# Optimization experiments

Hardware: AMD Instinct MI355X
Metric: run time of the kernel (lower is better)

The kernel has to match this reference:

```python
import jax, jax.numpy as jnp
import numpy as np

N = 131072   # number of profile points
S = 64       # n_samples (PSF samples per point)
D = H = W = 256


def setup_inputs() -> dict:
    key = jax.random.key(0)
    k1, k2, k3, k4, k5, k6 = jax.random.split(key, 6)
    x = jax.random.normal(k1, (1, 1, D, H, W), dtype=jnp.float32)
    # voxel-space coordinates (x, y, z) inside the volume
    sampleGrid = jax.random.uniform(k2, (N, 3), dtype=jnp.float32) * jnp.array(
        [W - 1, H - 1, D - 1], dtype=jnp.float32)
    # small axis-angle rotations + translations: [N, 1, 6]
    rot = jax.random.normal(k3, (N, 1, 3), dtype=jnp.float32) * 0.02
    trn = jax.random.normal(k4, (N, 1, 3), dtype=jnp.float32) * 2.0
    ax = jnp.concatenate([rot, trn], axis=-1)
    half = jax.random.uniform(k5, (N, 1, 3), minval=1.0, maxval=3.0, dtype=jnp.float32)
    bound = jnp.concatenate([-half, half], axis=1)  # [N, 2, 3]
    InvCovScaled = jnp.eye(3, dtype=jnp.float32) * 0.5
    # torch.randn(...) - 0.5 from the original forward, hoisted out for determinism
    xyz_psf = jax.random.normal(k6, (N, S, 3), dtype=jnp.float32) - 0.5
    return dict(x=x, sampleGrid=sampleGrid, ax=ax, bound=bound,
                InvCovScaled=InvCovScaled, xyz_psf=xyz_psf)


def _axisangle2mat(a):
    # a: [N, 6] -> [N, 3, 4] = [R | t] via Rodrigues
    v, t = a[:, :3], a[:, 3:]
    theta = jnp.linalg.norm(v, axis=-1, keepdims=True)          # [N,1]
    k = v / jnp.maximum(theta, 1e-12)                            # unit axis
    kx, ky, kz = k[:, 0], k[:, 1], k[:, 2]
    z = jnp.zeros_like(kx)
    K = jnp.stack([z, -kz, ky, kz, z, -kx, -ky, kx, z], axis=-1).reshape(-1, 3, 3)
    ct = jnp.cos(theta)[..., None]  # [N,1,1]
    st = jnp.sin(theta)[..., None]
    I = jnp.eye(3, dtype=a.dtype)
    R = I + st * K + (1.0 - ct) * jnp.matmul(K, K)
    return jnp.concatenate([R, t[..., None]], axis=-1)           # [N,3,4]


def _grid_sample_3d(vol, grid):
    # vol: [D,H,W]; grid: [M,3] normalized coords (x,y,z) in [-1,1]
    # matches F.grid_sample(mode='bilinear', padding_mode='zeros', align_corners=False)
    d, h, w = vol.shape
    sizes = jnp.array([w, h, d], dtype=vol.dtype)
    pix = ((grid + 1.0) * sizes - 1.0) * 0.5                     # unnormalize
    ix, iy, iz = pix[:, 0], pix[:, 1], pix[:, 2]
    x0 = jnp.floor(ix); y0 = jnp.floor(iy); z0 = jnp.floor(iz)
    fx = ix - x0; fy = iy - y0; fz = iz - z0
    x0 = x0.astype(jnp.int32); y0 = y0.astype(jnp.int32); z0 = z0.astype(jnp.int32)

    def gather(xi, yi, zi):
        valid = ((xi >= 0) & (xi < w) & (yi >= 0) & (yi < h) & (zi >= 0) & (zi < d))
        xc = jnp.clip(xi, 0, w - 1)
        yc = jnp.clip(yi, 0, h - 1)
        zc = jnp.clip(zi, 0, d - 1)
        return jnp.where(valid, vol[zc, yc, xc], jnp.zeros((), vol.dtype))

    out = jnp.zeros(grid.shape[0], dtype=vol.dtype)
    for dx in (0, 1):
        wx = fx if dx else (1.0 - fx)
        for dy in (0, 1):
            wy = fy if dy else (1.0 - fy)
            for dz in (0, 1):
                wz = fz if dz else (1.0 - fz)
                out = out + gather(x0 + dx, y0 + dy, z0 + dz) * (wx * wy * wz)
    return out


def reference(x, sampleGrid, ax, bound, InvCovScaled, xyz_psf):
    vol = x[0, 0]                                                # [D,H,W]
    size = jnp.array([x.shape[-1], x.shape[-2], x.shape[-3]], dtype=x.dtype)  # [W,H,D]

    # pose matrices [N,1,3,4]
    mat = _axisangle2mat(ax.reshape(-1, 6)).reshape(ax.shape[:-1] + (3, 4))
    R = mat[..., :3]                                             # [N,1,3,3]
    T = mat[..., 3]                                              # [N,1,3]
    # trans_first=True: p' = R @ (p + T)
    p = sampleGrid[:, None] + T                                  # [N,1,3]
    mat_sampleGrid = jnp.einsum('nkij,nkj->nki', R, p)           # [N,1,3]

    # PSF offsets: [N,S,3]
    bound_psf = xyz_psf * ((bound[:, 1, :] - bound[:, 0, :]) * 0.5)[:, None]
    psf = mat_sampleGrid + bound_psf                             # [N,S,3]

    grid = 2.0 * (psf / (size - 1.0) - 0.5)                      # normalize per-axis
    psf_x = _grid_sample_3d(vol, grid.reshape(-1, 3)).reshape(psf.shape[:-1])  # [N,S]

    center = bound_psf
    q = jnp.einsum('nsi,ij,nsj->ns', center, InvCovScaled, center)
    w = jnp.exp(-0.5 * q)                                        # [N,S]
    y = (psf_x * w).sum(-1) / w.sum(-1)                          # [N]
    return y
```

## Files before the change

### kernel.cpp

```cpp
#include <hip/hip_runtime.h>


#define VOL_N 256
#define S_PSF 64
#define NBUCKET 4096
#define TBL_ELEMS (1 << 24)
#define TBL_BYTES ((size_t)TBL_ELEMS * 8)

typedef float vf4 __attribute__((ext_vector_type(4)));
typedef _Float16 vh4 __attribute__((ext_vector_type(4)));
typedef _Float16 vh8 __attribute__((ext_vector_type(8)));


__device__ __forceinline__ int bucket_of(const float* __restrict__ sg, int n) {
    int cx = min(max((int)sg[n * 3 + 0], 0), VOL_N - 1) >> 4;
    int cy = min(max((int)sg[n * 3 + 1], 0), VOL_N - 1) >> 4;
    int cz = min(max((int)sg[n * 3 + 2], 0), VOL_N - 1) >> 4;
    int m = 0;
    #pragma unroll
    for (int b = 0; b < 4; b++) {
        m |= (((cx >> b) & 1) << (3 * b))
           | (((cy >> b) & 1) << (3 * b + 1))
           | (((cz >> b) & 1) << (3 * b + 2));
    }
    return m;
}

__global__ void zero_hist_kernel(int* __restrict__ ws) {
    int i = blockIdx.x * blockDim.x + threadIdx.x;
    if (i < NBUCKET) ws[i] = 0;
}

__global__ void hist_kernel(const float* __restrict__ sg, int* __restrict__ ws, int N) {
    int n = blockIdx.x * blockDim.x + threadIdx.x;
    if (n >= N) return;
    atomicAdd(&ws[bucket_of(sg, n)], 1);
}

__global__ __launch_bounds__(1024) void scan_kernel(int* __restrict__ ws) {
    __shared__ int tmp[1024];
    const int t = threadIdx.x;
    int h0 = ws[t * 4 + 0], h1 = ws[t * 4 + 1], h2 = ws[t * 4 + 2], h3 = ws[t * 4 + 3];
    int s = h0 + h1 + h2 + h3;
    tmp[t] = s;
    __syncthreads();
    for (int off = 1; off < 1024; off <<= 1) {
        int v = (t >= off) ? tmp[t - off] : 0;
        __syncthreads();
        tmp[t] += v;
        __syncthreads();
    }
    int excl = tmp[t] - s;
    ws[NBUCKET + t * 4 + 0] = excl;
    ws[NBUCKET + t * 4 + 1] = excl + h0;
    ws[NBUCKET + t * 4 + 2] = excl + h0 + h1;
    ws[NBUCKET + t * 4 + 3] = excl + h0 + h1 + h2;
}

__global__ void scatter_kernel(const float* __restrict__ sg,
                               const float* __restrict__ ax,
                               const float* __restrict__ bound,
                               int* __restrict__ ws,
                               float* __restrict__ pre, int N) {
    int n = blockIdx.x * blockDim.x + threadIdx.x;
    if (n >= N) return;
    int b = bucket_of(sg, n);
    int pos = atomicAdd(&ws[NBUCKET + b], 1);
    ws[2 * NBUCKET + pos] = n;

    const float vx = ax[n * 6 + 0], vy = ax[n * 6 + 1], vz = ax[n * 6 + 2];
    const float tx = ax[n * 6 + 3], ty = ax[n * 6 + 4], tz = ax[n * 6 + 5];

    const float theta = sqrtf(vx * vx + vy * vy + vz * vz);
    const float kinv = 1.0f / fmaxf(theta, 1e-12f);
    const float kx = vx * kinv, ky = vy * kinv, kz = vz * kinv;
    const float ct = __cosf(theta), st = __sinf(theta);
    const float oc = 1.0f - ct;

    const float r00 = 1.0f + oc * (-(ky * ky + kz * kz));
    const float r01 = -st * kz + oc * kx * ky;
    const float r02 =  st * ky + oc * kx * kz;
    const float r10 =  st * kz + oc * kx * ky;
    const float r11 = 1.0f + oc * (-(kx * kx + kz * kz));
    const float r12 = -st * kx + oc * ky * kz;
    const float r20 = -st * ky + oc * kx * kz;
    const float r21 =  st * kx + oc * ky * kz;
    const float r22 = 1.0f + oc * (-(kx * kx + ky * ky));

    const float px = sg[n * 3 + 0] + tx;
    const float py = sg[n * 3 + 1] + ty;
    const float pz = sg[n * 3 + 2] + tz;

    const float cx = r00 * px + r01 * py + r02 * pz;
    const float cy = r10 * px + r11 * py + r12 * pz;
    const float cz = r20 * px + r21 * py + r22 * pz;

    const float hx = (bound[n * 6 + 3] - bound[n * 6 + 0]) * 0.5f;
    const float hy = (bound[n * 6 + 4] - bound[n * 6 + 1]) * 0.5f;
    const float hz = (bound[n * 6 + 5] - bound[n * 6 + 2]) * 0.5f;

    const float scale = (float)VOL_N / (float)(VOL_N - 1);
    float4 A = make_float4(cx * scale - 0.5f, cy * scale - 0.5f,
                           cz * scale - 0.5f, hx);
    float4 B = make_float4(hy, hz, 0.0f, 0.0f);
    *(float4*)(pre + (size_t)pos * 8)     = A;
    *(float4*)(pre + (size_t)pos * 8 + 4) = B;
}

__global__ __launch_bounds__(256) void build_quad_kernel(
    const float* __restrict__ vol, vh4* __restrict__ tbl) {
    const int t = blockIdx.x * 256 + threadIdx.x;
    const int x2 = (t & 127) << 1;
    const int y = (t >> 7) & 255;
    const int z = t >> 15;
    const float* r0 = vol + (z << 16) + (y << 8);
    const float* r1 = vol + (z << 16) + (min(y + 1, VOL_N - 1) << 8);
    const float2 a = *(const float2*)(r0 + x2);
    const float2 b = *(const float2*)(r1 + x2);
    const float a2 = (x2 == VOL_N - 2) ? a.y : r0[x2 + 2];
    const float b2 = (x2 == VOL_N - 2) ? b.y : r1[x2 + 2];

    union { vh8 h; vf4 f; } o;
    o.h = (vh8){(_Float16)a.x, (_Float16)a.y, (_Float16)b.x, (_Float16)b.y,
                (_Float16)a.y, (_Float16)a2,  (_Float16)b.y, (_Float16)b2};
    *(vf4*)(tbl + ((z << 16) + (y << 8) + x2)) = o.f;
}

template <bool USE_TBL, bool USE_PRE>
__global__ __launch_bounds__(256, 4) void psf_sample_kernel(
    const float* __restrict__ vol,
    const vh4* __restrict__ tbl,
    const float* __restrict__ sampleGrid,
    const float* __restrict__ ax,
    const float* __restrict__ bound,
    const float* __restrict__ invcov,
    const float* __restrict__ xyz_psf,
    const int* __restrict__ perm,
    const float* __restrict__ pre,
    float* __restrict__ out,
    int N)
{
    const int lane = threadIdx.x & 63;

    int bid = blockIdx.x;
    const int nb = gridDim.x;
    if ((nb & 7) == 0) bid = (bid & 7) * (nb >> 3) + (bid >> 3);

    const int ii = bid * (blockDim.x >> 6) + (threadIdx.x >> 6);
    if (ii >= N) return;
    const int i = __builtin_amdgcn_readfirstlane(ii);
    const int n = USE_PRE ? __builtin_amdgcn_readfirstlane(perm[i]) : i;

    const float scale = (float)VOL_N / (float)(VOL_N - 1);
    float icx, icy, icz, hx, hy, hz;
    if (USE_PRE) {
        const float4 A = *(const float4*)(pre + (size_t)i * 8);
        const float4 B = *(const float4*)(pre + (size_t)i * 8 + 4);
        icx = A.x; icy = A.y; icz = A.z; hx = A.w; hy = B.x; hz = B.y;
    } else {
        const float vx = ax[n * 6 + 0], vy = ax[n * 6 + 1], vz = ax[n * 6 + 2];
        const float tx = ax[n * 6 + 3], ty = ax[n * 6 + 4], tz = ax[n * 6 + 5];
        const float theta = sqrtf(vx * vx + vy * vy + vz * vz);
        const float kinv = 1.0f / fmaxf(theta, 1e-12f);
        const float kx = vx * kinv, ky = vy * kinv, kz = vz * kinv;
        const float ct = __cosf(theta), st = __sinf(theta);
        const float oc = 1.0f - ct;
        const float r00 = 1.0f + oc * (-(ky * ky + kz * kz));
        const float r01 = -st * kz + oc * kx * ky;
        const float r02 =  st * ky + oc * kx * kz;
        const float r10 =  st * kz + oc * kx * ky;
        const float r11 = 1.0f + oc * (-(kx * kx + kz * kz));
        const float r12 = -st * kx + oc * ky * kz;
        const float r20 = -st * ky + oc * kx * kz;
        const float r21 =  st * kx + oc * ky * kz;
        const float r22 = 1.0f + oc * (-(kx * kx + ky * ky));
        const float px = sampleGrid[n * 3 + 0] + tx;
        const float py = sampleGrid[n * 3 + 1] + ty;
        const float pz = sampleGrid[n * 3 + 2] + tz;
        icx = (r00 * px + r01 * py + r02 * pz) * scale - 0.5f;
        icy = (r10 * px + r11 * py + r12 * pz) * scale - 0.5f;
        icz = (r20 * px + r21 * py + r22 * pz) * scale - 0.5f;
        hx = (bound[n * 6 + 3] - bound[n * 6 + 0]) * 0.5f;
        hy = (bound[n * 6 + 4] - bound[n * 6 + 1]) * 0.5f;
        hz = (bound[n * 6 + 5] - bound[n * 6 + 2]) * 0.5f;
    }

    const float m00 = invcov[0], m01 = invcov[1], m02 = invcov[2];
    const float m10 = invcov[3], m11 = invcov[4], m12 = invcov[5];
    const float m20 = invcov[6], m21 = invcov[7], m22 = invcov[8];

    const int pbase = (n * S_PSF + lane) * 3;
    const float gx = __builtin_nontemporal_load(xyz_psf + pbase + 0);
    const float gy = __builtin_nontemporal_load(xyz_psf + pbase + 1);
    const float gz = __builtin_nontemporal_load(xyz_psf + pbase + 2);
    const float ox = gx * hx, oy = gy * hy, oz = gz * hz;

    const float ix = fmaf(ox, scale, icx);
    const float iy = fmaf(oy, scale, icy);
    const float iz = fmaf(oz, scale, icz);

    const float x0f = floorf(ix), y0f = floorf(iy), z0f = floorf(iz);
    const float fx = ix - x0f, fy = iy - y0f, fz = iz - z0f;
    const int x0 = (int)x0f, y0 = (int)y0f, z0 = (int)z0f;

    const float wx0 = ((unsigned)x0       < (unsigned)VOL_N) ? (1.0f - fx) : 0.0f;
    const float wx1 = ((unsigned)(x0 + 1) < (unsigned)VOL_N) ? fx          : 0.0f;
    const float wy0 = ((unsigned)y0       < (unsigned)VOL_N) ? (1.0f - fy) : 0.0f;
    const float wy1 = ((unsigned)(y0 + 1) < (unsigned)VOL_N) ? fy          : 0.0f;
    const float wz0 = ((unsigned)z0       < (unsigned)VOL_N) ? (1.0f - fz) : 0.0f;
    const float wz1 = ((unsigned)(z0 + 1) < (unsigned)VOL_N) ? fz          : 0.0f;

    float v000, v001, v010, v011, v100, v101, v110, v111;
    if (USE_TBL) {
        const int xg = min(max(x0, 0), VOL_N - 1);
        const int yg = min(max(y0, 0), VOL_N - 1);
        const int zg0 = min(max(z0, 0), VOL_N - 1);
        const int zg1 = min(max(z0 + 1, 0), VOL_N - 1);
        const int common = (yg << 8) + xg;
        const vh4 p0 = tbl[(zg0 << 16) + common];
        const vh4 p1 = tbl[(zg1 << 16) + common];
        const bool lox = x0 < 0;
        const bool loy = y0 < 0;
        float s00 = p0.x, s01 = p0.y, s10 = p0.z, s11 = p0.w;
        float a01 = lox ? s00 : s01, a11 = lox ? s10 : s11;
        v000 = s00;                 v001 = a01;
        v010 = loy ? s00 : s10;     v011 = loy ? a01 : a11;
        s00 = p1.x; s01 = p1.y; s10 = p1.z; s11 = p1.w;
        a01 = lox ? s00 : s01; a11 = lox ? s10 : s11;
        v100 = s00;                 v101 = a01;
        v110 = loy ? s00 : s10;     v111 = loy ? a01 : a11;
    } else {
        const int xc0 = min(max(x0, 0), VOL_N - 1);
        const int xc1 = min(max(x0 + 1, 0), VOL_N - 1);
        const int yc0 = min(max(y0, 0), VOL_N - 1);
        const int yc1 = min(max(y0 + 1, 0), VOL_N - 1);
        const int zc0 = min(max(z0, 0), VOL_N - 1);
        const int zc1 = min(max(z0 + 1, 0), VOL_N - 1);
        const int zo0 = zc0 << 16, zo1 = zc1 << 16;
        const int yo0 = yc0 << 8, yo1 = yc1 << 8;
        v000 = vol[zo0 + yo0 + xc0];
        v001 = vol[zo0 + yo0 + xc1];
        v010 = vol[zo0 + yo1 + xc0];
        v011 = vol[zo0 + yo1 + xc1];
        v100 = vol[zo1 + yo0 + xc0];
        v101 = vol[zo1 + yo0 + xc1];
        v110 = vol[zo1 + yo1 + xc0];
        v111 = vol[zo1 + yo1 + xc1];
    }

    const float r0 = fmaf(v001, wx1, v000 * wx0);
    const float r1 = fmaf(v011, wx1, v010 * wx0);
    const float r2 = fmaf(v101, wx1, v100 * wx0);
    const float r3 = fmaf(v111, wx1, v110 * wx0);
    const float s0 = fmaf(r1, wy1, r0 * wy0);
    const float s1 = fmaf(r3, wy1, r2 * wy0);
    const float acc = fmaf(s1, wz1, s0 * wz0);

    const float qx = fmaf(m00, ox, fmaf(m01, oy, m02 * oz));
    const float qy = fmaf(m10, ox, fmaf(m11, oy, m12 * oz));
    const float qz = fmaf(m20, ox, fmaf(m21, oy, m22 * oz));
    const float q = fmaf(ox, qx, fmaf(oy, qy, oz * qz));
    const float w = __expf(-0.5f * q);

    float num = acc * w;
    float den = w;
    #pragma unroll
    for (int m = 32; m >= 1; m >>= 1) {
        num += __shfl_xor(num, m, 64);
        den += __shfl_xor(den, m, 64);
    }
    if (lane == 0) out[n] = num / den;
}

extern "C" void kernel_launch(void* const* d_in, const int* in_sizes, int n_in,
                              void* d_out, int out_size, void* d_ws, size_t ws_size,
                              hipStream_t stream) {
    const float* x        = (const float*)d_in[0];
    const float* sg       = (const float*)d_in[1];
    const float* ax       = (const float*)d_in[2];
    const float* bound    = (const float*)d_in[3];
    const float* invcov   = (const float*)d_in[4];
    const float* xyz_psf  = (const float*)d_in[5];
    float* out            = (float*)d_out;

    const int N = in_sizes[1] / 3;
    const size_t sort_bytes = (size_t)(2 * NBUCKET + N) * sizeof(int);
    const size_t sort_pad   = (sort_bytes + 31) & ~(size_t)31;
    const size_t pre_bytes  = (size_t)N * 8 * sizeof(float);

    const bool use_tbl  = ws_size >= TBL_BYTES + sort_pad + pre_bytes;
    const bool use_sort = use_tbl || ws_size >= sort_pad + pre_bytes;

    vh4* tbl = use_tbl ? (vh4*)d_ws : nullptr;
    char* base = (char*)d_ws + (use_tbl ? TBL_BYTES : 0);
    int* sort_ws = (int*)base;
    float* pre = (float*)(base + sort_pad);

    int* perm = nullptr;
    if (use_sort) {
        zero_hist_kernel<<<(NBUCKET + 255) / 256, 256, 0, stream>>>(sort_ws);
        hist_kernel<<<(N + 255) / 256, 256, 0, stream>>>(sg, sort_ws, N);
        scan_kernel<<<1, 1024, 0, stream>>>(sort_ws);
        scatter_kernel<<<(N + 255) / 256, 256, 0, stream>>>(sg, ax, bound, sort_ws, pre, N);
        perm = sort_ws + 2 * NBUCKET;
    }
    if (use_tbl) {
        build_quad_kernel<<<(VOL_N * VOL_N * VOL_N / 2) / 256, 256, 0, stream>>>(x, tbl);
    }

    dim3 block(256);
    dim3 grid((N + 3) / 4);
    if (use_tbl) {
        psf_sample_kernel<true, true><<<grid, block, 0, stream>>>(
            x, tbl, sg, ax, bound, invcov, xyz_psf, perm, pre, out, N);
    } else if (use_sort) {
        psf_sample_kernel<false, true><<<grid, block, 0, stream>>>(
            x, nullptr, sg, ax, bound, invcov, xyz_psf, perm, pre, out, N);
    } else {
        psf_sample_kernel<false, false><<<grid, block, 0, stream>>>(
            x, nullptr, sg, ax, bound, invcov, xyz_psf, nullptr, nullptr, out, N);
    }
}
```

Baseline: 304.3 us.

## Process four points per wavefront with 16 lanes each and vectorised PSF loads

```diff
diff --git a/kernel.cpp b/kernel.cpp
--- a/kernel.cpp
+++ b/kernel.cpp
@@ -126,13 +126,10 @@
     *(vf4*)(tbl + ((z << 16) + (y << 8) + x2)) = o.f;
 }
 
-template <bool USE_TBL, bool USE_PRE>
-__global__ __launch_bounds__(256, 4) void psf_sample_kernel(
+template <bool USE_TBL>
+__global__ __launch_bounds__(256, 4) void psf_sample_g4_kernel(
     const float* __restrict__ vol,
     const vh4* __restrict__ tbl,
-    const float* __restrict__ sampleGrid,
-    const float* __restrict__ ax,
-    const float* __restrict__ bound,
     const float* __restrict__ invcov,
     const float* __restrict__ xyz_psf,
     const int* __restrict__ perm,
@@ -141,64 +138,177 @@
     int N)
 {
     const int lane = threadIdx.x & 63;
+    const int g = lane >> 4;
+    const int t = lane & 15;
 
     int bid = blockIdx.x;
     const int nb = gridDim.x;
     if ((nb & 7) == 0) bid = (bid & 7) * (nb >> 3) + (bid >> 3);
 
-    const int ii = bid * (blockDim.x >> 6) + (threadIdx.x >> 6);
-    if (ii >= N) return;
-    const int i = __builtin_amdgcn_readfirstlane(ii);
-    const int n = USE_PRE ? __builtin_amdgcn_readfirstlane(perm[i]) : i;
-
-    const float scale = (float)VOL_N / (float)(VOL_N - 1);
-    float icx, icy, icz, hx, hy, hz;
-    if (USE_PRE) {
-        const float4 A = *(const float4*)(pre + (size_t)i * 8);
-        const float4 B = *(const float4*)(pre + (size_t)i * 8 + 4);
-        icx = A.x; icy = A.y; icz = A.z; hx = A.w; hy = B.x; hz = B.y;
-    } else {
-        const float vx = ax[n * 6 + 0], vy = ax[n * 6 + 1], vz = ax[n * 6 + 2];
-        const float tx = ax[n * 6 + 3], ty = ax[n * 6 + 4], tz = ax[n * 6 + 5];
-        const float theta = sqrtf(vx * vx + vy * vy + vz * vz);
-        const float kinv = 1.0f / fmaxf(theta, 1e-12f);
-        const float kx = vx * kinv, ky = vy * kinv, kz = vz * kinv;
-        const float ct = __cosf(theta), st = __sinf(theta);
-        const float oc = 1.0f - ct;
-        const float r00 = 1.0f + oc * (-(ky * ky + kz * kz));
-        const float r01 = -st * kz + oc * kx * ky;
-        const float r02 =  st * ky + oc * kx * kz;
-        const float r10 =  st * kz + oc * kx * ky;
-        const float r11 = 1.0f + oc * (-(kx * kx + kz * kz));
-        const float r12 = -st * kx + oc * ky * kz;
-        const float r20 = -st * ky + oc * kx * kz;
-        const float r21 =  st * kx + oc * ky * kz;
-        const float r22 = 1.0f + oc * (-(kx * kx + ky * ky));
-        const float px = sampleGrid[n * 3 + 0] + tx;
-        const float py = sampleGrid[n * 3 + 1] + ty;
-        const float pz = sampleGrid[n * 3 + 2] + tz;
-        icx = (r00 * px + r01 * py + r02 * pz) * scale - 0.5f;
-        icy = (r10 * px + r11 * py + r12 * pz) * scale - 0.5f;
-        icz = (r20 * px + r21 * py + r22 * pz) * scale - 0.5f;
-        hx = (bound[n * 6 + 3] - bound[n * 6 + 0]) * 0.5f;
-        hy = (bound[n * 6 + 4] - bound[n * 6 + 1]) * 0.5f;
-        hz = (bound[n * 6 + 5] - bound[n * 6 + 2]) * 0.5f;
-    }
+    const int wave = threadIdx.x >> 6;
+    const int i = (bid * 4 + wave) * 4 + g;
+    const bool valid = i < N;
+    const int ic = valid ? i : 0;
+    const int n = perm[ic];
+
+    const float4 A = *(const float4*)(pre + (size_t)ic * 8);
+    const float4 B = *(const float4*)(pre + (size_t)ic * 8 + 4);
+    const float icx = A.x, icy = A.y, icz = A.z;
+    const float hx = A.w, hy = B.x, hz = B.y;
 
     const float m00 = invcov[0], m01 = invcov[1], m02 = invcov[2];
     const float m10 = invcov[3], m11 = invcov[4], m12 = invcov[5];
     const float m20 = invcov[6], m21 = invcov[7], m22 = invcov[8];
 
+    const float* pp = xyz_psf + ((size_t)n * (S_PSF * 3) + t * 12);
+    const vf4 f0 = __builtin_nontemporal_load((const vf4*)pp);
+    const vf4 f1 = __builtin_nontemporal_load((const vf4*)pp + 1);
+    const vf4 f2 = __builtin_nontemporal_load((const vf4*)pp + 2);
+
+    const float gxx[4] = {f0.x, f0.w, f1.z, f2.y};
+    const float gyy[4] = {f0.y, f1.x, f1.w, f2.z};
+    const float gzz[4] = {f0.z, f1.y, f2.x, f2.w};
+
+    const float scale = (float)VOL_N / (float)(VOL_N - 1);
+    float num = 0.0f, den = 0.0f;
+
+    #pragma unroll
+    for (int k = 0; k < 4; ++k) {
+        const float ox = gxx[k] * hx, oy = gyy[k] * hy, oz = gzz[k] * hz;
+
+        const float ix = fmaf(ox, scale, icx);
+        const float iy = fmaf(oy, scale, icy);
+        const float iz = fmaf(oz, scale, icz);
+
+        const float x0f = floorf(ix), y0f = floorf(iy), z0f = floorf(iz);
+        const float fx = ix - x0f, fy = iy - y0f, fz = iz - z0f;
+        const int x0 = (int)x0f, y0 = (int)y0f, z0 = (int)z0f;
+
+        const float wx0 = ((unsigned)x0       < (unsigned)VOL_N) ? (1.0f - fx) : 0.0f;
+        const float wx1 = ((unsigned)(x0 + 1) < (unsigned)VOL_N) ? fx          : 0.0f;
+        const float wy0 = ((unsigned)y0       < (unsigned)VOL_N) ? (1.0f - fy) : 0.0f;
+        const float wy1 = ((unsigned)(y0 + 1) < (unsigned)VOL_N) ? fy          : 0.0f;
+        const float wz0 = ((unsigned)z0       < (unsigned)VOL_N) ? (1.0f - fz) : 0.0f;
+        const float wz1 = ((unsigned)(z0 + 1) < (unsigned)VOL_N) ? fz          : 0.0f;
+
+        float v000, v001, v010, v011, v100, v101, v110, v111;
+        if (USE_TBL) {
+            const int xg = min(max(x0, 0), VOL_N - 1);
+            const int yg = min(max(y0, 0), VOL_N - 1);
+            const int zg0 = min(max(z0, 0), VOL_N - 1);
+            const int zg1 = min(max(z0 + 1, 0), VOL_N - 1);
+            const int common = (yg << 8) + xg;
+            const vh4 p0 = tbl[(zg0 << 16) + common];
+            const vh4 p1 = tbl[(zg1 << 16) + common];
+            const bool lox = x0 < 0;
+            const bool loy = y0 < 0;
+            float s00 = p0.x, s01 = p0.y, s10 = p0.z, s11 = p0.w;
+            float a01 = lox ? s00 : s01, a11 = lox ? s10 : s11;
+            v000 = s00;                 v001 = a01;
+            v010 = loy ? s00 : s10;     v011 = loy ? a01 : a11;
+            s00 = p1.x; s01 = p1.y; s10 = p1.z; s11 = p1.w;
+            a01 = lox ? s00 : s01; a11 = lox ? s10 : s11;
+            v100 = s00;                 v101 = a01;
+            v110 = loy ? s00 : s10;     v111 = loy ? a01 : a11;
+        } else {
+            const int xc0 = min(max(x0, 0), VOL_N - 1);
+            const int xc1 = min(max(x0 + 1, 0), VOL_N - 1);
+            const int yc0 = min(max(y0, 0), VOL_N - 1);
+            const int yc1 = min(max(y0 + 1, 0), VOL_N - 1);
+            const int zc0 = min(max(z0, 0), VOL_N - 1);
+            const int zc1 = min(max(z0 + 1, 0), VOL_N - 1);
+            const int zo0 = zc0 << 16, zo1 = zc1 << 16;
+            const int yo0 = yc0 << 8, yo1 = yc1 << 8;
+            v000 = vol[zo0 + yo0 + xc0];
+            v001 = vol[zo0 + yo0 + xc1];
+            v010 = vol[zo0 + yo1 + xc0];
+            v011 = vol[zo0 + yo1 + xc1];
+            v100 = vol[zo1 + yo0 + xc0];
+            v101 = vol[zo1 + yo0 + xc1];
+            v110 = vol[zo1 + yo1 + xc0];
+            v111 = vol[zo1 + yo1 + xc1];
+        }
+
+        const float r0 = fmaf(v001, wx1, v000 * wx0);
+        const float r1 = fmaf(v011, wx1, v010 * wx0);
+        const float r2 = fmaf(v101, wx1, v100 * wx0);
+        const float r3 = fmaf(v111, wx1, v110 * wx0);
+        const float s0 = fmaf(r1, wy1, r0 * wy0);
+        const float s1 = fmaf(r3, wy1, r2 * wy0);
+        const float acc = fmaf(s1, wz1, s0 * wz0);
+
+        const float qx = fmaf(m00, ox, fmaf(m01, oy, m02 * oz));
+        const float qy = fmaf(m10, ox, fmaf(m11, oy, m12 * oz));
+        const float qz = fmaf(m20, ox, fmaf(m21, oy, m22 * oz));
+        const float q = fmaf(ox, qx, fmaf(oy, qy, oz * qz));
+        const float w = __expf(-0.5f * q);
+
+        num = fmaf(acc, w, num);
+        den += w;
+    }
+
+    #pragma unroll
+    for (int m = 8; m >= 1; m >>= 1) {
+        num += __shfl_xor(num, m, 64);
+        den += __shfl_xor(den, m, 64);
+    }
+    if (t == 0 && valid) out[n] = num / den;
+}
+
+__global__ __launch_bounds__(256, 4) void psf_sample_plain_kernel(
+    const float* __restrict__ vol,
+    const float* __restrict__ sampleGrid,
+    const float* __restrict__ ax,
+    const float* __restrict__ bound,
+    const float* __restrict__ invcov,
+    const float* __restrict__ xyz_psf,
+    float* __restrict__ out,
+    int N)
+{
+    const int lane = threadIdx.x & 63;
+    const int i = blockIdx.x * (blockDim.x >> 6) + (threadIdx.x >> 6);
+    if (i >= N) return;
+    const int n = __builtin_amdgcn_readfirstlane(i);
+
+    const float vx = ax[n * 6 + 0], vy = ax[n * 6 + 1], vz = ax[n * 6 + 2];
+    const float tx = ax[n * 6 + 3], ty = ax[n * 6 + 4], tz = ax[n * 6 + 5];
+    const float theta = sqrtf(vx * vx + vy * vy + vz * vz);
+    const float kinv = 1.0f / fmaxf(theta, 1e-12f);
+    const float kx = vx * kinv, ky = vy * kinv, kz = vz * kinv;
+    const float ct = __cosf(theta), st = __sinf(theta);
+    const float oc = 1.0f - ct;
+    const float r00 = 1.0f + oc * (-(ky * ky + kz * kz));
+    const float r01 = -st * kz + oc * kx * ky;
+    const float r02 =  st * ky + oc * kx * kz;
+    const float r10 =  st * kz + oc * kx * ky;
+    const float r11 = 1.0f + oc * (-(kx * kx + kz * kz));
+    const float r12 = -st * kx + oc * ky * kz;
+    const float r20 = -st * ky + oc * kx * kz;
+    const float r21 =  st * kx + oc * ky * kz;
+    const float r22 = 1.0f + oc * (-(kx * kx + ky * ky));
+    const float px = sampleGrid[n * 3 + 0] + tx;
+    const float py = sampleGrid[n * 3 + 1] + ty;
+    const float pz = sampleGrid[n * 3 + 2] + tz;
+    const float scale = (float)VOL_N / (float)(VOL_N - 1);
+    const float icx = (r00 * px + r01 * py + r02 * pz) * scale - 0.5f;
+    const float icy = (r10 * px + r11 * py + r12 * pz) * scale - 0.5f;
+    const float icz = (r20 * px + r21 * py + r22 * pz) * scale - 0.5f;
+    const float hx = (bound[n * 6 + 3] - bound[n * 6 + 0]) * 0.5f;
+    const float hy = (bound[n * 6 + 4] - bound[n * 6 + 1]) * 0.5f;
+    const float hz = (bound[n * 6 + 5] - bound[n * 6 + 2]) * 0.5f;
+
+    const float m00 = invcov[0], m01 = invcov[1], m02 = invcov[2];
+    const float m10 = invcov[3], m11 = invcov[4], m12 = invcov[5];
+    const float m20 = invcov[6], m21 = invcov[7], m22 = invcov[8];
+
     const int pbase = (n * S_PSF + lane) * 3;
-    const float gx = __builtin_nontemporal_load(xyz_psf + pbase + 0);
-    const float gy = __builtin_nontemporal_load(xyz_psf + pbase + 1);
-    const float gz = __builtin_nontemporal_load(xyz_psf + pbase + 2);
-    const float ox = gx * hx, oy = gy * hy, oz = gz * hz;
+    const float ox = xyz_psf[pbase + 0] * hx;
+    const float oy = xyz_psf[pbase + 1] * hy;
+    const float oz = xyz_psf[pbase + 2] * hz;
 
     const float ix = fmaf(ox, scale, icx);
     const float iy = fmaf(oy, scale, icy);
     const float iz = fmaf(oz, scale, icz);
-
     const float x0f = floorf(ix), y0f = floorf(iy), z0f = floorf(iz);
     const float fx = ix - x0f, fy = iy - y0f, fz = iz - z0f;
     const int x0 = (int)x0f, y0 = (int)y0f, z0 = (int)z0f;
@@ -210,43 +320,22 @@
     const float wz0 = ((unsigned)z0       < (unsigned)VOL_N) ? (1.0f - fz) : 0.0f;
     const float wz1 = ((unsigned)(z0 + 1) < (unsigned)VOL_N) ? fz          : 0.0f;
 
-    float v000, v001, v010, v011, v100, v101, v110, v111;
-    if (USE_TBL) {
-        const int xg = min(max(x0, 0), VOL_N - 1);
-        const int yg = min(max(y0, 0), VOL_N - 1);
-        const int zg0 = min(max(z0, 0), VOL_N - 1);
-        const int zg1 = min(max(z0 + 1, 0), VOL_N - 1);
-        const int common = (yg << 8) + xg;
-        const vh4 p0 = tbl[(zg0 << 16) + common];
-        const vh4 p1 = tbl[(zg1 << 16) + common];
-        const bool lox = x0 < 0;
-        const bool loy = y0 < 0;
-        float s00 = p0.x, s01 = p0.y, s10 = p0.z, s11 = p0.w;
-        float a01 = lox ? s00 : s01, a11 = lox ? s10 : s11;
-        v000 = s00;                 v001 = a01;
-        v010 = loy ? s00 : s10;     v011 = loy ? a01 : a11;
-        s00 = p1.x; s01 = p1.y; s10 = p1.z; s11 = p1.w;
-        a01 = lox ? s00 : s01; a11 = lox ? s10 : s11;
-        v100 = s00;                 v101 = a01;
-        v110 = loy ? s00 : s10;     v111 = loy ? a01 : a11;
-    } else {
-        const int xc0 = min(max(x0, 0), VOL_N - 1);
-        const int xc1 = min(max(x0 + 1, 0), VOL_N - 1);
-        const int yc0 = min(max(y0, 0), VOL_N - 1);
-        const int yc1 = min(max(y0 + 1, 0), VOL_N - 1);
-        const int zc0 = min(max(z0, 0), VOL_N - 1);
-        const int zc1 = min(max(z0 + 1, 0), VOL_N - 1);
-        const int zo0 = zc0 << 16, zo1 = zc1 << 16;
-        const int yo0 = yc0 << 8, yo1 = yc1 << 8;
-        v000 = vol[zo0 + yo0 + xc0];
-        v001 = vol[zo0 + yo0 + xc1];
-        v010 = vol[zo0 + yo1 + xc0];
-        v011 = vol[zo0 + yo1 + xc1];
-        v100 = vol[zo1 + yo0 + xc0];
-        v101 = vol[zo1 + yo0 + xc1];
-        v110 = vol[zo1 + yo1 + xc0];
-        v111 = vol[zo1 + yo1 + xc1];
-    }
+    const int xc0 = min(max(x0, 0), VOL_N - 1);
+    const int xc1 = min(max(x0 + 1, 0), VOL_N - 1);
+    const int yc0 = min(max(y0, 0), VOL_N - 1);
+    const int yc1 = min(max(y0 + 1, 0), VOL_N - 1);
+    const int zc0 = min(max(z0, 0), VOL_N - 1);
+    const int zc1 = min(max(z0 + 1, 0), VOL_N - 1);
+    const int zo0 = zc0 << 16, zo1 = zc1 << 16;
+    const int yo0 = yc0 << 8, yo1 = yc1 << 8;
+    const float v000 = vol[zo0 + yo0 + xc0];
+    const float v001 = vol[zo0 + yo0 + xc1];
+    const float v010 = vol[zo0 + yo1 + xc0];
+    const float v011 = vol[zo0 + yo1 + xc1];
+    const float v100 = vol[zo1 + yo0 + xc0];
+    const float v101 = vol[zo1 + yo0 + xc1];
+    const float v110 = vol[zo1 + yo1 + xc0];
+    const float v111 = vol[zo1 + yo1 + xc1];
 
     const float r0 = fmaf(v001, wx1, v000 * wx0);
     const float r1 = fmaf(v011, wx1, v010 * wx0);
@@ -308,16 +397,20 @@
         build_quad_kernel<<<(VOL_N * VOL_N * VOL_N / 2) / 256, 256, 0, stream>>>(x, tbl);
     }
 
-    dim3 block(256);
-    dim3 grid((N + 3) / 4);
-    if (use_tbl) {
-        psf_sample_kernel<true, true><<<grid, block, 0, stream>>>(
-            x, tbl, sg, ax, bound, invcov, xyz_psf, perm, pre, out, N);
-    } else if (use_sort) {
-        psf_sample_kernel<false, true><<<grid, block, 0, stream>>>(
-            x, nullptr, sg, ax, bound, invcov, xyz_psf, perm, pre, out, N);
+    if (use_sort) {
+        dim3 block(256);
+        dim3 grid((N + 15) / 16);
+        if (use_tbl) {
+            psf_sample_g4_kernel<true><<<grid, block, 0, stream>>>(
+                x, tbl, invcov, xyz_psf, perm, pre, out, N);
+        } else {
+            psf_sample_g4_kernel<false><<<grid, block, 0, stream>>>(
+                x, nullptr, invcov, xyz_psf, perm, pre, out, N);
+        }
     } else {
-        psf_sample_kernel<false, false><<<grid, block, 0, stream>>>(
-            x, nullptr, sg, ax, bound, invcov, xyz_psf, nullptr, nullptr, out, N);
-    }
-}
+        dim3 block(256);
+        dim3 grid((N + 3) / 4);
+        psf_sample_plain_kernel<<<grid, block, 0, stream>>>(
+            x, sg, ax, bound, invcov, xyz_psf, out, N);
+    }
+}
```

After: 339.9 us. +11.7%, slower.
